# Optimization experiments

Hardware: AMD Instinct MI355X
Metric: run time of the kernel (lower is better)

## Reference

```python
import jax, jax.numpy as jnp
import numpy as np

N = 100000       # nodes
E = 1600000      # edges
NFEAT, NHID, NCLASS = 512, 256, 40
NLAYERS = 10     # APPNP propagation steps K
ALPHA = 0.1      # teleport probability


def setup_inputs() -> dict:
    key = jax.random.key(0)
    ks = jax.random.split(key, 8)
    x = jax.random.normal(ks[0], (N, NFEAT), jnp.float32)
    row = jax.random.randint(ks[1], (E,), 0, N, jnp.int32)
    col = jax.random.randint(ks[2], (E,), 0, N, jnp.int32)
    vals = jax.random.uniform(ks[3], (E,), jnp.float32)
    # MyLinear init: uniform(-stdv, stdv) with stdv = 1/sqrt(in_features);
    # bias is a shape-[1] scalar (faithful to torch.FloatTensor([out_features])).
    s1 = 1.0 / np.sqrt(NFEAT)
    s2 = 1.0 / np.sqrt(NHID)
    W1 = jax.random.uniform(ks[4], (NFEAT, NHID), jnp.float32, -s1, s1)
    b1 = jax.random.uniform(ks[5], (1,), jnp.float32, -s1, s1)
    W2 = jax.random.uniform(ks[6], (NHID, NCLASS), jnp.float32, -s2, s2)
    b2 = jax.random.uniform(ks[7], (1,), jnp.float32, -s2, s2)
    return dict(x=x, row=row, col=col, vals=vals, W1=W1, b1=b1, W2=W2, b2=b2)


def reference(x, row, col, vals, W1, b1, W2, b2):
    # 2-layer MLP (eval mode: dropout inactive, no BN)
    h = jax.nn.relu(x @ W1 + b1)          # [N, NHID]
    h = h @ W2 + b2                        # [N, NCLASS]

    # sparse adjacency spmm via edge-list segment sum
    def spmm(z):
        return jax.ops.segment_sum(vals[:, None] * z[col], row, num_segments=N)

    # APPNP propagation: z <- (1-alpha) * A z + alpha * h
    def step(z, _):
        z = (1.0 - ALPHA) * spmm(z) + ALPHA * h
        return z, None

    z, _ = jax.lax.scan(step, h, None, length=NLAYERS)
    return jax.nn.log_softmax(z, axis=1)
```

## Files before the change

kernel.cpp:

```cpp
#include <hip/hip_runtime.h>


typedef unsigned short ushort_t;
typedef short short8 __attribute__((ext_vector_type(8)));
typedef float f32x4 __attribute__((ext_vector_type(4)));

#define NFEAT 512
#define NHID 256
#define NCLASS 40

static __device__ __forceinline__ float b2f(ushort_t u) {
    unsigned v = ((unsigned)u) << 16;
    float f;
    __builtin_memcpy(&f, &v, 4);
    return f;
}
static __device__ __forceinline__ ushort_t f2b(float f) {
    unsigned u;
    __builtin_memcpy(&u, &f, 4);
    unsigned r = u + 0x7FFFu + ((u >> 16) & 1u);
    return (ushort_t)(r >> 16);
}
static __device__ __forceinline__ ushort_t san_u(ushort_t u) {
    return ((u & 0x7F80u) == 0x7F80u) ? (ushort_t)0 : u;
}
static __device__ __forceinline__ float ldmix(const void* p, size_t i, int isbf) {
    if (isbf) return b2f(san_u(((const ushort_t*)p)[i]));
    return ((const float*)p)[i];
}
static __device__ __forceinline__ void stz(void* p, size_t i, int zbf, float v) {
    if (zbf) ((ushort_t*)p)[i] = f2b(v);
    else ((float*)p)[i] = v;
}

static __device__ __forceinline__ void gld_lds16(const ushort_t* g, ushort_t* l) {
    __builtin_amdgcn_global_load_lds(
        (const __attribute__((address_space(1))) unsigned int*)g,
        (__attribute__((address_space(3))) unsigned int*)l, 16, 0, 0);
}

__global__ void detect_kernel(const ushort_t* __restrict__ x, int* __restrict__ flag) {
    __shared__ int cnt_s;
    if (threadIdx.x == 0) cnt_s = 0;
    __syncthreads();
    int c = 0;
    for (int i = threadIdx.x; i < 2048; i += 256) {
        ushort_t u = x[2 * i];
        int e = (u >> 7) & 0xFF;
        if (e >= 107 && e <= 141) c++;
    }
    atomicAdd(&cnt_s, c);
    __syncthreads();
    if (threadIdx.x == 0) flag[0] = (cnt_s >= 1024) ? 1 : 0;
}


__global__ void zero_kernel(int* __restrict__ p, int n) {
    int i = blockIdx.x * 256 + threadIdx.x;
    if (i < n) p[i] = 0;
}

__global__ void hist_kernel(const int* __restrict__ row, int* __restrict__ deg, int e, int n) {
    int i = blockIdx.x * 256 + threadIdx.x;
    if (i < e) {
        int r = row[i];
        if ((unsigned)r < (unsigned)n) atomicAdd(&deg[r], 1);
    }
}

__global__ void scan_blocksum(const int* __restrict__ deg, int* __restrict__ bsum, int n) {
    __shared__ int s[256];
    int t = threadIdx.x;
    int i = blockIdx.x * 256 + t;
    s[t] = (i < n) ? deg[i] : 0;
    __syncthreads();
    for (int o = 128; o; o >>= 1) {
        if (t < o) s[t] += s[t + o];
        __syncthreads();
    }
    if (t == 0) bsum[blockIdx.x] = s[0];
}

__global__ void scan_bsum_excl(int* __restrict__ bsum, int nb) {
    __shared__ int s[512];
    int t = threadIdx.x;
    int v = (t < nb) ? bsum[t] : 0;
    int own = v;
    s[t] = v;
    __syncthreads();
    for (int o = 1; o < 512; o <<= 1) {
        int add = (t >= o) ? s[t - o] : 0;
        __syncthreads();
        s[t] += add;
        __syncthreads();
    }
    if (t < nb) bsum[t] = s[t] - own;
}

__global__ void scan_emit(const int* __restrict__ deg, const int* __restrict__ bsum,
                          int* __restrict__ row_start, int* __restrict__ cursor, int n) {
    __shared__ int s[256];
    int t = threadIdx.x;
    int i = blockIdx.x * 256 + t;
    int v = (i < n) ? deg[i] : 0;
    int own = v;
    s[t] = v;
    __syncthreads();
    for (int o = 1; o < 256; o <<= 1) {
        int add = (t >= o) ? s[t - o] : 0;
        __syncthreads();
        s[t] += add;
        __syncthreads();
    }
    if (i < n) {
        int rs = bsum[blockIdx.x] + s[t] - own;
        row_start[i] = rs;
        cursor[i] = rs;
    }
}

__global__ void scatter_kernel(const int* __restrict__ row, const int* __restrict__ col,
                               const void* __restrict__ vals, int* __restrict__ cursor,
                               int2* __restrict__ cs, const int* __restrict__ flag, int e,
                               int n, int nshard) {
    int shard = blockIdx.x & 7;
    int i = (blockIdx.x >> 3) * 256 + threadIdx.x;
    if (i >= e) return;
    int r = row[i];
    if ((unsigned)r >= (unsigned)n) return;
    int s0 = shard * nshard;
    if (r < s0 || r >= s0 + nshard) return;
    int isbf = flag[0];
    int p = atomicAdd(&cursor[r], 1);
    if ((unsigned)p < (unsigned)e) {
        int c = col[i];
        float v = ldmix(vals, i, isbf);
        int2 rec;
        rec.x = ((unsigned)c < (unsigned)n) ? c : 0;
        __builtin_memcpy(&rec.y, &v, 4);
        cs[p] = rec;
    }
}


__global__ void w1frag_kernel(const void* __restrict__ W1, ushort_t* __restrict__ w1f,
                              const int* __restrict__ flag) {
    int t = blockIdx.x * 256 + threadIdx.x;
    if (t >= 16 * 16 * 64) return;
    int isbf = flag[0];
    int l = t & 63, nt = (t >> 6) & 15, kb = t >> 10;
    ushort_t tmp[8];
#pragma unroll
    for (int j = 0; j < 8; j++) {
        int k = kb * 32 + (l >> 4) * 8 + j;
        int nn = nt * 16 + (l & 15);
        tmp[j] = f2b(ldmix(W1, (size_t)k * NHID + nn, isbf));
    }
    *(short8*)(w1f + (size_t)t * 8) = *(short8*)tmp;
}

__global__ void w2frag_kernel(const void* __restrict__ W2, ushort_t* __restrict__ w2f,
                              const int* __restrict__ flag) {
    int t = blockIdx.x * 256 + threadIdx.x;
    if (t >= 8 * 3 * 64) return;
    int isbf = flag[0];
    int l = t % 64;
    int nt = (t / 64) % 3;
    int kb = t / 192;
    ushort_t tmp[8];
#pragma unroll
    for (int j = 0; j < 8; j++) {
        int k = kb * 32 + (l >> 4) * 8 + j;
        int nn = nt * 16 + (l & 15);
        tmp[j] = (nn < NCLASS) ? f2b(ldmix(W2, (size_t)k * NCLASS + nn, isbf)) : (ushort_t)0;
    }
    *(short8*)(w2f + (size_t)t * 8) = *(short8*)tmp;
}


template <int ISBF>
static __device__ __forceinline__ short8 load_afrag(const void* __restrict__ x, size_t base) {
    short8 av;
    if (ISBF) {
        av = *(const short8*)((const ushort_t*)x + base);
#pragma unroll
        for (int j = 0; j < 8; j++) {
            ushort_t u = (ushort_t)av[j];
            if ((u & 0x7F80u) == 0x7F80u) av[j] = 0;
        }
    } else {
        const float* xf = (const float*)x + base;
        f32x4 a0 = *(const f32x4*)xf;
        f32x4 a1 = *(const f32x4*)(xf + 4);
#pragma unroll
        for (int j = 0; j < 4; j++) {
            av[j] = (short)f2b(a0[j]);
            av[4 + j] = (short)f2b(a1[j]);
        }
    }
    return av;
}

#define APITCH 42

template <int ISBF>
static __device__ __forceinline__ void gemm1_staged(const void* __restrict__ x,
                                                    const ushort_t* __restrict__ w1f,
                                                    size_t xbase, ushort_t* Bl0, ushort_t* Bl1,
                                                    ushort_t* awr0, ushort_t* awr1,
                                                    const ushort_t* ard0, const ushort_t* ard1,
                                                    const ushort_t* brd0, const ushort_t* brd1,
                                                    f32x4 (&acc)[16], int wv, int l) {
    {
        short8 a0 = load_afrag<ISBF>(x, xbase);
        *(short8*)awr0 = a0;
        const ushort_t* src = w1f + (size_t)wv * 512 + (size_t)l * 8;
#pragma unroll
        for (int i = 0; i < 4; i++) gld_lds16(src + i * 2048, Bl0 + wv * 512 + i * 2048);
    }
    __syncthreads();

#pragma unroll
    for (int kb = 0; kb < 16; kb++) {
        const bool even = (kb & 1) == 0;
        const ushort_t* brd = even ? brd0 : brd1;
        const ushort_t* ard = even ? ard0 : ard1;
        ushort_t* awrn = even ? awr1 : awr0;
        ushort_t* bln = even ? Bl1 : Bl0;
        short8 an;
        if (kb < 15) {
            an = load_afrag<ISBF>(x, xbase + (size_t)(kb + 1) * 32);
            const ushort_t* src =
                w1f + (size_t)(kb + 1) * 8192 + (size_t)wv * 512 + (size_t)l * 8;
#pragma unroll
            for (int i = 0; i < 4; i++) gld_lds16(src + i * 2048, bln + wv * 512 + i * 2048);
        }
        short8 af = *(const short8*)ard;
#pragma unroll
        for (int nt = 0; nt < 16; nt++) {
            short8 bf = *(const short8*)(brd + nt * 512);
            acc[nt] = __builtin_amdgcn_mfma_f32_16x16x32_bf16(af, bf, acc[nt], 0, 0, 0);
        }
        if (kb < 15) *(short8*)awrn = an;
        __syncthreads();
    }
}

__global__ __launch_bounds__(256, 3) void mlp_kernel(const void* __restrict__ x,
                                                     const ushort_t* __restrict__ w1f,
                                                     const ushort_t* __restrict__ w2f,
                                                     const void* __restrict__ b1,
                                                     const void* __restrict__ b2,
                                                     void* __restrict__ h,
                                                     const int* __restrict__ flag, int zbf,
                                                     int n) {
    __shared__ __align__(16) ushort_t pool[21760];
    ushort_t* Bl0 = pool;
    ushort_t* Bl1 = pool + 8192;
    ushort_t* Al0 = pool + 16384;
    ushort_t* Al1 = pool + 16384 + 2688;
    ushort_t* Hl = pool;

    const int t = threadIdx.x;
    const int isbf = flag[0];
    const int wv = t >> 6, l = t & 63;
    const int lq = l >> 4, lr = l & 15;
    const int m0 = blockIdx.x * 64;

    const int rS = t >> 2, qS = t & 3;
    int rowS = m0 + rS;
    if (rowS > n - 1) rowS = n - 1;
    const size_t xbase = (size_t)rowS * NFEAT + (size_t)qS * 8;
    ushort_t* awr0 = Al0 + rS * APITCH + qS * 8;
    ushort_t* awr1 = Al1 + rS * APITCH + qS * 8;
    const ushort_t* ard0 = Al0 + (wv * 16 + lr) * APITCH + lq * 8;
    const ushort_t* ard1 = Al1 + (wv * 16 + lr) * APITCH + lq * 8;
    const ushort_t* brd0 = Bl0 + l * 8;
    const ushort_t* brd1 = Bl1 + l * 8;

    f32x4 acc[16];
#pragma unroll
    for (int i = 0; i < 16; i++) acc[i] = (f32x4){0.f, 0.f, 0.f, 0.f};

    if (isbf)
        gemm1_staged<1>(x, w1f, xbase, Bl0, Bl1, awr0, awr1, ard0, ard1, brd0, brd1, acc, wv, l);
    else
        gemm1_staged<0>(x, w1f, xbase, Bl0, Bl1, awr0, awr1, ard0, ard1, brd0, brd1, acc, wv, l);

    float bias1 = ldmix(b1, 0, isbf);
#pragma unroll
    for (int nt = 0; nt < 16; nt++) {
#pragma unroll
        for (int i = 0; i < 4; i++) {
            float v = acc[nt][i] + bias1;
            v = fmaxf(v, 0.f);
            Hl[(wv * 16 + lq * 4 + i) * 264 + nt * 16 + lr] = f2b(v);
        }
    }
    __syncthreads();

    f32x4 acc2[3];
#pragma unroll
    for (int i = 0; i < 3; i++) acc2[i] = (f32x4){0.f, 0.f, 0.f, 0.f};
    const ushort_t* hp = Hl + (wv * 16 + lr) * 264 + lq * 8;
#pragma unroll
    for (int kb = 0; kb < 8; kb++) {
        short8 afrag = *(const short8*)(hp + kb * 32);
#pragma unroll
        for (int nt = 0; nt < 3; nt++) {
            short8 bfrag = *(const short8*)(w2f + ((size_t)(kb * 3 + nt) * 64 + l) * 8);
            acc2[nt] = __builtin_amdgcn_mfma_f32_16x16x32_bf16(afrag, bfrag, acc2[nt], 0, 0, 0);
        }
    }

    float bias2 = ldmix(b2, 0, isbf);
#pragma unroll
    for (int nt = 0; nt < 3; nt++) {
#pragma unroll
        for (int i = 0; i < 4; i++) {
            int rowg = m0 + wv * 16 + lq * 4 + i;
            int colg = nt * 16 + lr;
            if (rowg < n && colg < NCLASS)
                stz(h, (size_t)rowg * NCLASS + colg, zbf, acc2[nt][i] + bias2);
        }
    }
}


__global__ __launch_bounds__(256) void prop_kernel(const void* __restrict__ zin,
                                                   void* __restrict__ zout,
                                                   const void* __restrict__ h,
                                                   const int* __restrict__ row_start,
                                                   const int* __restrict__ deg,
                                                   const int2* __restrict__ cs, int n) {
    int g = blockIdx.x * 4 + (threadIdx.x >> 6);
    int lane = threadIdx.x & 63;
    int a = g * 2, b = g * 2 + 1;
    if (a >= n) return;
    const bool hasb = (b < n);
    int sa = row_start[a], da = deg[a];
    int sb = hasb ? row_start[b] : 0;
    int db = hasb ? deg[b] : 0;
    const bool laneok = lane < NCLASS;
    const ushort_t* zi = (const ushort_t*)zin;
    float acca = 0.f, accb = 0.f;
    int dmax = (da > db) ? da : db;
    for (int base = 0; base < dmax; base += 64) {
        int ma = da - base;
        ma = (ma < 0) ? 0 : ((ma > 64) ? 64 : ma);
        int mb = db - base;
        mb = (mb < 0) ? 0 : ((mb > 64) ? 64 : mb);
        int ca = 0, cb = 0;
        float va = 0.f, vb = 0.f;
        if (lane < ma) {
            int2 r = cs[(size_t)sa + base + lane];
            ca = r.x;
            __builtin_memcpy(&va, &r.y, 4);
        }
        if (lane < mb) {
            int2 r = cs[(size_t)sb + base + lane];
            cb = r.x;
            __builtin_memcpy(&vb, &r.y, 4);
        }
        int mm = (ma > mb) ? ma : mb;
        for (int j = 0; j < mm; j += 8) {
            int cca[8], ccb[8];
            float vva[8], vvb[8];
#pragma unroll
            for (int k = 0; k < 8; k++) {
                cca[k] = __shfl(ca, j + k);
                vva[k] = __shfl(va, j + k);
                ccb[k] = __shfl(cb, j + k);
                vvb[k] = __shfl(vb, j + k);
            }
            if (laneok) {
                float zva[8], zvb[8];
#pragma unroll
                for (int k = 0; k < 8; k++) zva[k] = b2f(zi[(size_t)cca[k] * NCLASS + lane]);
#pragma unroll
                for (int k = 0; k < 8; k++) zvb[k] = b2f(zi[(size_t)ccb[k] * NCLASS + lane]);
#pragma unroll
                for (int k = 0; k < 8; k++) acca += vva[k] * zva[k];
#pragma unroll
                for (int k = 0; k < 8; k++) accb += vvb[k] * zvb[k];
            }
        }
    }
    if (laneok) {
        {
            float hv = b2f(((const ushort_t*)h)[(size_t)a * NCLASS + lane]);
            ((ushort_t*)zout)[(size_t)a * NCLASS + lane] = f2b(0.9f * acca + 0.1f * hv);
        }
        if (hasb) {
            float hv = b2f(((const ushort_t*)h)[(size_t)b * NCLASS + lane]);
            ((ushort_t*)zout)[(size_t)b * NCLASS + lane] = f2b(0.9f * accb + 0.1f * hv);
        }
    }
}


__global__ __launch_bounds__(256) void lsm_kernel(const void* __restrict__ z,
                                                  void* __restrict__ out,
                                                  const int* __restrict__ flag, int n) {
    int w = blockIdx.x * 4 + (threadIdx.x >> 6);
    int lane = threadIdx.x & 63;
    if (w >= n) return;
    int isbf = flag[0];
    float v = (lane < NCLASS) ? b2f(((const ushort_t*)z)[(size_t)w * NCLASS + lane]) : -INFINITY;
    float m = v;
    for (int o = 32; o; o >>= 1) m = fmaxf(m, __shfl_xor(m, o));
    float e = (lane < NCLASS) ? __expf(v - m) : 0.f;
    float s = e;
    for (int o = 32; o; o >>= 1) s += __shfl_xor(s, o);
    if (lane < NCLASS) {
        float r = v - m - __logf(s);
        if (isbf) ((ushort_t*)out)[(size_t)w * NCLASS + lane] = f2b(r);
        else ((float*)out)[(size_t)w * NCLASS + lane] = r;
    }
}


extern "C" void kernel_launch(void* const* d_in, const int* in_sizes, int n_in, void* d_out,
                              int out_size, void* d_ws, size_t ws_size, hipStream_t stream) {
    const void* x = d_in[0];
    const int* row = (const int*)d_in[1];
    const int* col = (const int*)d_in[2];
    const void* vals = d_in[3];
    const void* W1 = d_in[4];
    const void* b1 = d_in[5];
    const void* W2 = d_in[6];
    const void* b2 = d_in[7];

    const int N = in_sizes[0] / NFEAT;
    const int E = in_sizes[1];

    const size_t ez = 2;

    char* ws = (char*)d_ws;
    size_t off = 0;
    auto take = [&](size_t bytes) {
        size_t o = off;
        off = (off + bytes + 255) & ~(size_t)255;
        return (void*)(ws + o);
    };
    void* h = take((size_t)N * NCLASS * ez);
    void* zA = take((size_t)N * NCLASS * ez);
    void* zB = take((size_t)N * NCLASS * ez);
    int2* cs = (int2*)take((size_t)E * 8);
    int* deg = (int*)take((size_t)N * 4);
    int* row_start = (int*)take((size_t)N * 4);
    int* cursor = (int*)take((size_t)N * 4);
    ushort_t* w1f = (ushort_t*)take((size_t)NFEAT * NHID * 2);
    ushort_t* w2f = (ushort_t*)take((size_t)8 * 3 * 64 * 8 * 2);
    int* bsum = (int*)take(512 * 4);
    int* flag = (int*)take(256);

    const int NB = (N + 255) / 256;
    const int EB = (E + 255) / 256;
    const int GB = (N + 63) / 64;
    const int PB = (N + 3) / 4;
    const int NSHARD = (N + 7) / 8;
    const int PB2 = ((N + 1) / 2 + 3) / 4;

    detect_kernel<<<1, 256, 0, stream>>>((const ushort_t*)x, flag);

    zero_kernel<<<(N + 255) / 256, 256, 0, stream>>>(deg, N);
    hist_kernel<<<EB, 256, 0, stream>>>(row, deg, E, N);
    scan_blocksum<<<NB, 256, 0, stream>>>(deg, bsum, N);
    scan_bsum_excl<<<1, 512, 0, stream>>>(bsum, NB);
    scan_emit<<<NB, 256, 0, stream>>>(deg, bsum, row_start, cursor, N);
    scatter_kernel<<<EB * 8, 256, 0, stream>>>(row, col, vals, cursor, cs, flag, E, N, NSHARD);

    w1frag_kernel<<<64, 256, 0, stream>>>(W1, w1f, flag);
    w2frag_kernel<<<6, 256, 0, stream>>>(W2, w2f, flag);

    mlp_kernel<<<GB, 256, 0, stream>>>(x, w1f, w2f, b1, b2, h, flag, 1, N);

    prop_kernel<<<PB2, 256, 0, stream>>>(h, zA, h, row_start, deg, cs, N);
    {
        const void* zi = zA;
        void* zo = zB;
        for (int s = 1; s < 10; s++) {
            prop_kernel<<<PB2, 256, 0, stream>>>(zi, zo, h, row_start, deg, cs, N);
            const void* tmp = zi;
            zi = zo;
            zo = (void*)tmp;
        }
        lsm_kernel<<<PB, 256, 0, stream>>>(zi, d_out, flag, N);
    }
}
```

Measured before the change: 1.004 ms.

## Split each row's edges across three lane groups with packed bf16x2 gathers

The propagation kernel now gives one wavefront per node instead of two. It splits the node's edges into three contiguous chunks, one per group of 20 lanes, and each lane gathers a 32-bit word holding two bf16 classes. The three partial sums are combined with shuffles before the teleport mix and a packed store. This uses 60 of 64 lanes instead of 40 and halves the gather instructions per edge. The cost is more per-lane edge-record loads (each lane loads its own record, not a shuffle broadcast) and a cross-group reduction.

```diff
diff --git a/kernel.cpp b/kernel.cpp
--- a/kernel.cpp
+++ b/kernel.cpp
@@ -2,6 +2,7 @@
 
 
 typedef unsigned short ushort_t;
+typedef unsigned int uint_t;
 typedef short short8 __attribute__((ext_vector_type(8)));
 typedef float f32x4 __attribute__((ext_vector_type(4)));
 
@@ -333,68 +334,67 @@
                                                    const int* __restrict__ row_start,
                                                    const int* __restrict__ deg,
                                                    const int2* __restrict__ cs, int n) {
-    int g = blockIdx.x * 4 + (threadIdx.x >> 6);
+    int w = blockIdx.x * 4 + (threadIdx.x >> 6);
     int lane = threadIdx.x & 63;
-    int a = g * 2, b = g * 2 + 1;
-    if (a >= n) return;
-    const bool hasb = (b < n);
-    int sa = row_start[a], da = deg[a];
-    int sb = hasb ? row_start[b] : 0;
-    int db = hasb ? deg[b] : 0;
-    const bool laneok = lane < NCLASS;
-    const ushort_t* zi = (const ushort_t*)zin;
-    float acca = 0.f, accb = 0.f;
-    int dmax = (da > db) ? da : db;
-    for (int base = 0; base < dmax; base += 64) {
-        int ma = da - base;
-        ma = (ma < 0) ? 0 : ((ma > 64) ? 64 : ma);
-        int mb = db - base;
-        mb = (mb < 0) ? 0 : ((mb > 64) ? 64 : mb);
-        int ca = 0, cb = 0;
-        float va = 0.f, vb = 0.f;
-        if (lane < ma) {
-            int2 r = cs[(size_t)sa + base + lane];
-            ca = r.x;
-            __builtin_memcpy(&va, &r.y, 4);
-        }
-        if (lane < mb) {
-            int2 r = cs[(size_t)sb + base + lane];
-            cb = r.x;
-            __builtin_memcpy(&vb, &r.y, 4);
-        }
-        int mm = (ma > mb) ? ma : mb;
-        for (int j = 0; j < mm; j += 8) {
-            int cca[8], ccb[8];
-            float vva[8], vvb[8];
-#pragma unroll
-            for (int k = 0; k < 8; k++) {
-                cca[k] = __shfl(ca, j + k);
-                vva[k] = __shfl(va, j + k);
-                ccb[k] = __shfl(cb, j + k);
-                vvb[k] = __shfl(vb, j + k);
-            }
-            if (laneok) {
-                float zva[8], zvb[8];
-#pragma unroll
-                for (int k = 0; k < 8; k++) zva[k] = b2f(zi[(size_t)cca[k] * NCLASS + lane]);
-#pragma unroll
-                for (int k = 0; k < 8; k++) zvb[k] = b2f(zi[(size_t)ccb[k] * NCLASS + lane]);
-#pragma unroll
-                for (int k = 0; k < 8; k++) acca += vva[k] * zva[k];
-#pragma unroll
-                for (int k = 0; k < 8; k++) accb += vvb[k] * zvb[k];
-            }
-        }
-    }
-    if (laneok) {
-        {
-            float hv = b2f(((const ushort_t*)h)[(size_t)a * NCLASS + lane]);
-            ((ushort_t*)zout)[(size_t)a * NCLASS + lane] = f2b(0.9f * acca + 0.1f * hv);
-        }
-        if (hasb) {
-            float hv = b2f(((const ushort_t*)h)[(size_t)b * NCLASS + lane]);
-            ((ushort_t*)zout)[(size_t)b * NCLASS + lane] = f2b(0.9f * accb + 0.1f * hv);
-        }
+    if (w >= n) return;
+    int start = row_start[w];
+    int d = deg[w];
+    const uint_t* zu = (const uint_t*)zin;
+
+    int g = lane / 20;
+    int cls2 = lane % 20;
+    int d3 = (d + 2) / 3;
+    int st = g * d3;
+    int len = d - st;
+    if (len < 0) len = 0;
+    if (len > d3) len = d3;
+    if (g >= 3) len = 0;
+    int safebase = start;
+
+    float acc0 = 0.f, acc1 = 0.f;
+    for (int base = 0; base < d3; base += 8) {
+        int2 rec[8];
+#pragma unroll
+        for (int q = 0; q < 8; q++) {
+            int e = base + q;
+            int ee = (e < len) ? e : ((len > 0) ? (len - 1) : 0);
+            int idx = (len > 0) ? (start + st + ee) : safebase;
+            rec[q] = cs[(size_t)idx];
+        }
+        uint_t zd[8];
+        float vv[8];
+#pragma unroll
+        for (int q = 0; q < 8; q++) {
+            float v;
+            __builtin_memcpy(&v, &rec[q].y, 4);
+            vv[q] = ((base + q) < len) ? v : 0.f;
+            zd[q] = zu[(size_t)rec[q].x * 20 + cls2];
+        }
+#pragma unroll
+        for (int q = 0; q < 8; q++) {
+            uint_t ulo = zd[q] << 16;
+            uint_t uhi = zd[q] & 0xFFFF0000u;
+            float lo, hi;
+            __builtin_memcpy(&lo, &ulo, 4);
+            __builtin_memcpy(&hi, &uhi, 4);
+            acc0 += vv[q] * lo;
+            acc1 += vv[q] * hi;
+        }
+    }
+
+    float s0 = acc0 + __shfl(acc0, lane + 20) + __shfl(acc0, lane + 40);
+    float s1 = acc1 + __shfl(acc1, lane + 20) + __shfl(acc1, lane + 40);
+
+    if (lane < 20) {
+        uint_t hu = ((const uint_t*)h)[(size_t)w * 20 + lane];
+        uint_t hlo = hu << 16, hhi = hu & 0xFFFF0000u;
+        float h0, h1;
+        __builtin_memcpy(&h0, &hlo, 4);
+        __builtin_memcpy(&h1, &hhi, 4);
+        float r0 = 0.9f * s0 + 0.1f * h0;
+        float r1 = 0.9f * s1 + 0.1f * h1;
+        uint_t outw = (uint_t)f2b(r0) | ((uint_t)f2b(r1) << 16);
+        ((uint_t*)zout)[(size_t)w * 20 + lane] = outw;
     }
 }
 
@@ -460,7 +460,6 @@
     const int GB = (N + 63) / 64;
     const int PB = (N + 3) / 4;
     const int NSHARD = (N + 7) / 8;
-    const int PB2 = ((N + 1) / 2 + 3) / 4;
 
     detect_kernel<<<1, 256, 0, stream>>>((const ushort_t*)x, flag);
 
@@ -476,12 +475,12 @@
 
     mlp_kernel<<<GB, 256, 0, stream>>>(x, w1f, w2f, b1, b2, h, flag, 1, N);
 
-    prop_kernel<<<PB2, 256, 0, stream>>>(h, zA, h, row_start, deg, cs, N);
+    prop_kernel<<<PB, 256, 0, stream>>>(h, zA, h, row_start, deg, cs, N);
     {
         const void* zi = zA;
         void* zo = zB;
         for (int s = 1; s < 10; s++) {
-            prop_kernel<<<PB2, 256, 0, stream>>>(zi, zo, h, row_start, deg, cs, N);
+            prop_kernel<<<PB, 256, 0, stream>>>(zi, zo, h, row_start, deg, cs, N);
             const void* tmp = zi;
             zi = zo;
             zo = (void*)tmp;
```

After: 943.7 us. -6.0%, faster.
